# Kernel optimization log

Hardware: AMD Instinct MI355X
Metric: run time of the kernel (lower is better)

## Reference

```python
import jax, jax.numpy as jnp
import numpy as np

B, C, H, W = 1, 1, 1024, 1024
NP = 16                    # n_patches
S = NP * NP                # 256 tokens
D = 2048                   # hidden_d
NH = 16                    # heads
DH = D // NH               # 128
MLP = 4 * D
NB = 2                     # blocks
INPUT_D = C * (H // NP) * (W // NP)  # 4096
EPS = 1e-5


def positional_embeddings(s, d):
    # result[i,j] = sin(i/10000**(j/d)) if j even else cos(i/10000**((j-1)/d))
    i = jnp.arange(s, dtype=jnp.float32)[:, None]
    j = jnp.arange(d, dtype=jnp.float32)[None, :]
    even = (jnp.arange(d) % 2 == 0)[None, :]
    expo = jnp.where(even, j, j - 1.0) / d
    ang = i / (10000.0 ** expo)
    return jnp.where(even, jnp.sin(ang), jnp.cos(ang))


def layer_norm(x, g, b):
    m = x.mean(-1, keepdims=True)
    v = ((x - m) ** 2).mean(-1, keepdims=True)
    return (x - m) / jnp.sqrt(v + EPS) * g + b


def setup_inputs() -> dict:
    key = jax.random.key(0)
    ks = jax.random.split(key, 20)
    s = 0.02
    return {
        "images": jax.random.normal(ks[0], (B, C, H, W), jnp.float32),
        "memory": jax.random.normal(ks[1], (1, 8), jnp.float32),
        "wmap": jax.random.normal(ks[2], (INPUT_D, D), jnp.float32) * s,
        "bmap": jnp.zeros((D,), jnp.float32),
        "ln1_g": jnp.ones((NB, D), jnp.float32),
        "ln1_b": jnp.zeros((NB, D), jnp.float32),
        "qw": jax.random.normal(ks[3], (NB, NH, DH, DH), jnp.float32) * s,
        "qb": jnp.zeros((NB, NH, DH), jnp.float32),
        "kw": jax.random.normal(ks[4], (NB, NH, DH, DH), jnp.float32) * s,
        "kb": jnp.zeros((NB, NH, DH), jnp.float32),
        "vw": jax.random.normal(ks[5], (NB, NH, DH, DH), jnp.float32) * s,
        "vb": jnp.zeros((NB, NH, DH), jnp.float32),
        "ln2_g": jnp.ones((NB, D), jnp.float32),
        "ln2_b": jnp.zeros((NB, D), jnp.float32),
        "w1": jax.random.normal(ks[6], (NB, D, MLP), jnp.float32) * s,
        "b1": jnp.zeros((NB, MLP), jnp.float32),
        "w2": jax.random.normal(ks[7], (NB, MLP, D), jnp.float32) * s,
        "b2": jnp.zeros((NB, D), jnp.float32),
        "head_w": jax.random.normal(ks[8], (D, 1), jnp.float32) * s,
        "head_b": jnp.zeros((1,), jnp.float32),
    }


def reference(images, memory, wmap, bmap, ln1_g, ln1_b, qw, qb, kw, kb, vw, vb,
              ln2_g, ln2_b, w1, b1, w2, b2, head_w, head_b):
    # patchify: view(1, n_patches**2, num_h*num_v) -> (1, 256, 4096)
    patches = images.reshape(1, S, INPUT_D)
    tokens = patches @ wmap + bmap                      # (1, S, D)
    x = tokens + positional_embeddings(S, D)
    scale = DH ** 0.5
    for l in range(NB):
        h = layer_norm(x, ln1_g[l], ln1_b[l])
        h4 = h.reshape(B, S, NH, DH)
        q = jnp.einsum('bshd,hde->bshe', h4, qw[l]) + qb[l]
        k = jnp.einsum('bshd,hde->bshe', h4, kw[l]) + kb[l]
        v = jnp.einsum('bshd,hde->bshe', h4, vw[l]) + vb[l]
        att = jax.nn.softmax(jnp.einsum('bshe,bthe->bhst', q, k) / scale, axis=-1)
        attn_out = jnp.einsum('bhst,bthe->bshe', att, v).reshape(B, S, D)
        x = x + attn_out
        h2 = layer_norm(x, ln2_g[l], ln2_b[l])
        x = x + (jax.nn.gelu(h2 @ w1[l] + b1[l], approximate=False) @ w2[l] + b2[l])
    cls = x[:, 0]                                       # (1, D)
    out = jax.nn.sigmoid(cls @ head_w + head_b)         # (1, 1)
    return (out, memory)
```

## Files before the change

kernel.cpp:

```cpp
#include <hip/hip_runtime.h>
#include <math.h>

#define SQ   256
#define DD   2048
#define NHD  16
#define DHD  128
#define MLPD 8192
#define KIN  4096
#define INV_SQRT_DH 0.08838834764831845f

typedef __attribute__((ext_vector_type(8))) short bf16x8;
typedef __attribute__((ext_vector_type(4))) float f32x4;

__device__ __forceinline__ float gelu_f(float x) {
    return 0.5f * x * (1.0f + erff(x * 0.70710678118654752f));
}

__device__ __forceinline__ short f2bf(float f) {
    unsigned u = __float_as_uint(f);
    unsigned r = (u + 0x7fffu + ((u >> 16) & 1u)) >> 16;
    return (short)r;
}

__global__ __launch_bounds__(256) void gemm_splitk(const float* __restrict__ A,
                                                   const float* __restrict__ W,
                                                   float* __restrict__ C,
                                                   int N, int K, int KC) {
    __shared__ short As[64 * 64];
    __shared__ short Bs[64 * 64];
    const int tid = threadIdx.x;
    const int n0 = blockIdx.x * 64, m0 = blockIdx.y * 64;
    const int kstart = blockIdx.z * KC;
    const int wv = tid >> 6, ln = tid & 63;
    const int l15 = ln & 15, q = ln >> 4;

    f32x4 acc[4];
    #pragma unroll
    for (int j = 0; j < 4; j++) acc[j] = (f32x4){0.f, 0.f, 0.f, 0.f};

    const int am = tid >> 2, akb = (tid & 3) * 16, ac0 = (tid & 3) * 2;
    const int bn = tid & 63, bkb = (tid >> 6) * 16, bc0 = (tid >> 6) * 2;
    short* as0 = &As[am * 64 + ((ac0 ^ (am & 7)) * 8)];
    short* as1 = &As[am * 64 + (((ac0 + 1) ^ (am & 7)) * 8)];
    short* bs0 = &Bs[bn * 64 + ((bc0 ^ (bn & 7)) * 8)];
    short* bs1 = &Bs[bn * 64 + (((bc0 + 1) ^ (bn & 7)) * 8)];
    const int arow = 16 * wv + l15;
    const short* af0 = &As[arow * 64 + ((q ^ (arow & 7)) * 8)];
    const short* af1 = &As[arow * 64 + (((q + 4) ^ (arow & 7)) * 8)];

    for (int kc = kstart; kc < kstart + KC; kc += 64) {
        const float* ap = A + (size_t)(m0 + am) * K + kc + akb;
        float4 a0 = *(const float4*)ap;
        float4 a1 = *(const float4*)(ap + 4);
        float4 a2 = *(const float4*)(ap + 8);
        float4 a3 = *(const float4*)(ap + 12);
        const float* wp = W + (size_t)(kc + bkb) * N + n0 + bn;
        float wb[16];
        #pragma unroll
        for (int j = 0; j < 16; j++) wb[j] = wp[(size_t)j * N];

        __syncthreads();
        {
            short t[16] = {f2bf(a0.x), f2bf(a0.y), f2bf(a0.z), f2bf(a0.w),
                           f2bf(a1.x), f2bf(a1.y), f2bf(a1.z), f2bf(a1.w),
                           f2bf(a2.x), f2bf(a2.y), f2bf(a2.z), f2bf(a2.w),
                           f2bf(a3.x), f2bf(a3.y), f2bf(a3.z), f2bf(a3.w)};
            *(bf16x8*)as0 = *(bf16x8*)&t[0];
            *(bf16x8*)as1 = *(bf16x8*)&t[8];
            short u[16];
            #pragma unroll
            for (int j = 0; j < 16; j++) u[j] = f2bf(wb[j]);
            *(bf16x8*)bs0 = *(bf16x8*)&u[0];
            *(bf16x8*)bs1 = *(bf16x8*)&u[8];
        }
        __syncthreads();

        bf16x8 fa0 = *(const bf16x8*)af0;
        bf16x8 fa1 = *(const bf16x8*)af1;
        #pragma unroll
        for (int jt = 0; jt < 4; jt++) {
            const int brow = 16 * jt + l15;
            bf16x8 fb0 = *(const bf16x8*)&Bs[brow * 64 + ((q ^ (brow & 7)) * 8)];
            bf16x8 fb1 = *(const bf16x8*)&Bs[brow * 64 + (((q + 4) ^ (brow & 7)) * 8)];
            acc[jt] = __builtin_amdgcn_mfma_f32_16x16x32_bf16(fa0, fb0, acc[jt], 0, 0, 0);
            acc[jt] = __builtin_amdgcn_mfma_f32_16x16x32_bf16(fa1, fb1, acc[jt], 0, 0, 0);
        }
    }
    #pragma unroll
    for (int jt = 0; jt < 4; jt++) {
        const int n = n0 + 16 * jt + l15;
        #pragma unroll
        for (int i = 0; i < 4; i++) {
            const int m = m0 + 16 * wv + q * 4 + i;
            atomicAdd(&C[(size_t)m * N + n], acc[jt][i]);
        }
    }
}

__global__ __launch_bounds__(256) void epi_pos(float* __restrict__ x,
                                               const float* __restrict__ bmap) {
    const int idx = blockIdx.x * 256 + threadIdx.x;
    const int m = idx >> 11, n = idx & 2047;
    float val = x[idx] + bmap[n];
    float jf = (float)n;
    float expo = ((n & 1) ? (jf - 1.0f) : jf) * (1.0f / 2048.0f);
    float ang = (float)m * powf(10000.0f, -expo);
    x[idx] = val + ((n & 1) ? cosf(ang) : sinf(ang));
}

__global__ __launch_bounds__(256) void epi_gelu(float* __restrict__ y,
                                                const float* __restrict__ b1) {
    const int idx = blockIdx.x * 256 + threadIdx.x;
    y[idx] = gelu_f(y[idx] + b1[idx & 8191]);
}

__global__ __launch_bounds__(256) void epi_bias(float* __restrict__ x,
                                                const float* __restrict__ b2) {
    const int idx = blockIdx.x * 256 + threadIdx.x;
    x[idx] += b2[idx & 2047];
}

__global__ __launch_bounds__(256) void qkv_mfma(const float* __restrict__ h,
                                                const float* __restrict__ qw, const float* __restrict__ kw,
                                                const float* __restrict__ vw, const float* __restrict__ qb,
                                                const float* __restrict__ kb, const float* __restrict__ vb,
                                                float* __restrict__ q, float* __restrict__ k,
                                                float* __restrict__ v) {
    __shared__ short As[64 * 64];
    __shared__ short Bs[64 * 64];
    const int head = blockIdx.x, m0 = blockIdx.y * 64;
    const int type = blockIdx.z >> 1, n0 = (blockIdx.z & 1) * 64;
    const float* W; const float* B; float* O;
    if (type == 0)      { W = qw; B = qb; O = q; }
    else if (type == 1) { W = kw; B = kb; O = k; }
    else                { W = vw; B = vb; O = v; }
    W += (size_t)head * DHD * DHD;
    B += head * DHD;
    const int hoff = head * DHD;
    const int tid = threadIdx.x;
    const int wv = tid >> 6, ln = tid & 63;
    const int l15 = ln & 15, qq = ln >> 4;

    f32x4 acc[4];
    #pragma unroll
    for (int j = 0; j < 4; j++) acc[j] = (f32x4){0.f, 0.f, 0.f, 0.f};

    const int am = tid >> 2, akb = (tid & 3) * 16, ac0 = (tid & 3) * 2;
    const int bn = tid & 63, bkb = (tid >> 6) * 16, bc0 = (tid >> 6) * 2;
    short* as0 = &As[am * 64 + ((ac0 ^ (am & 7)) * 8)];
    short* as1 = &As[am * 64 + (((ac0 + 1) ^ (am & 7)) * 8)];
    short* bs0 = &Bs[bn * 64 + ((bc0 ^ (bn & 7)) * 8)];
    short* bs1 = &Bs[bn * 64 + (((bc0 + 1) ^ (bn & 7)) * 8)];
    const int arow = 16 * wv + l15;
    const short* af0 = &As[arow * 64 + ((qq ^ (arow & 7)) * 8)];
    const short* af1 = &As[arow * 64 + (((qq + 4) ^ (arow & 7)) * 8)];

    for (int kc = 0; kc < DHD; kc += 64) {
        const float* ap = h + (size_t)(m0 + am) * DD + hoff + kc + akb;
        float4 a0 = *(const float4*)ap;
        float4 a1 = *(const float4*)(ap + 4);
        float4 a2 = *(const float4*)(ap + 8);
        float4 a3 = *(const float4*)(ap + 12);
        const float* wp = W + (size_t)(kc + bkb) * DHD + n0 + bn;
        float wb[16];
        #pragma unroll
        for (int j = 0; j < 16; j++) wb[j] = wp[j * DHD];

        __syncthreads();
        {
            short t[16] = {f2bf(a0.x), f2bf(a0.y), f2bf(a0.z), f2bf(a0.w),
                           f2bf(a1.x), f2bf(a1.y), f2bf(a1.z), f2bf(a1.w),
                           f2bf(a2.x), f2bf(a2.y), f2bf(a2.z), f2bf(a2.w),
                           f2bf(a3.x), f2bf(a3.y), f2bf(a3.z), f2bf(a3.w)};
            *(bf16x8*)as0 = *(bf16x8*)&t[0];
            *(bf16x8*)as1 = *(bf16x8*)&t[8];
            short u[16];
            #pragma unroll
            for (int j = 0; j < 16; j++) u[j] = f2bf(wb[j]);
            *(bf16x8*)bs0 = *(bf16x8*)&u[0];
            *(bf16x8*)bs1 = *(bf16x8*)&u[8];
        }
        __syncthreads();

        bf16x8 fa0 = *(const bf16x8*)af0;
        bf16x8 fa1 = *(const bf16x8*)af1;
        #pragma unroll
        for (int jt = 0; jt < 4; jt++) {
            const int brow = 16 * jt + l15;
            bf16x8 fb0 = *(const bf16x8*)&Bs[brow * 64 + ((qq ^ (brow & 7)) * 8)];
            bf16x8 fb1 = *(const bf16x8*)&Bs[brow * 64 + (((qq + 4) ^ (brow & 7)) * 8)];
            acc[jt] = __builtin_amdgcn_mfma_f32_16x16x32_bf16(fa0, fb0, acc[jt], 0, 0, 0);
            acc[jt] = __builtin_amdgcn_mfma_f32_16x16x32_bf16(fa1, fb1, acc[jt], 0, 0, 0);
        }
    }
    #pragma unroll
    for (int jt = 0; jt < 4; jt++) {
        const int n = n0 + 16 * jt + l15;
        #pragma unroll
        for (int i = 0; i < 4; i++) {
            const int m = m0 + 16 * wv + qq * 4 + i;
            O[(size_t)m * DD + hoff + n] = acc[jt][i] + B[n];
        }
    }
}

__global__ __launch_bounds__(256) void ln_kernel(const float* __restrict__ xin,
                                                 const float* __restrict__ g,
                                                 const float* __restrict__ b,
                                                 float* __restrict__ out,
                                                 float* __restrict__ zbuf, int zn) {
    __shared__ float red[8];
    const int tid = threadIdx.x;
    for (int i = tid; i < zn; i += 256) zbuf[i] = 0.0f;
    const int row = blockIdx.x;
    const float* xr = xin + row * DD;
    float vals[8];
    float s = 0.0f;
    #pragma unroll
    for (int i = 0; i < 8; i++) { vals[i] = xr[tid + i * 256]; s += vals[i]; }
    #pragma unroll
    for (int o = 32; o > 0; o >>= 1) s += __shfl_down(s, o);
    if ((tid & 63) == 0) red[tid >> 6] = s;
    __syncthreads();
    if (tid == 0) red[4] = (red[0] + red[1] + red[2] + red[3]) * (1.0f / 2048.0f);
    __syncthreads();
    const float mean = red[4];
    float vs = 0.0f;
    #pragma unroll
    for (int i = 0; i < 8; i++) { float d = vals[i] - mean; vs += d * d; }
    #pragma unroll
    for (int o = 32; o > 0; o >>= 1) vs += __shfl_down(vs, o);
    if ((tid & 63) == 0) red[tid >> 6] = vs;
    __syncthreads();
    if (tid == 0) red[5] = rsqrtf((red[0] + red[1] + red[2] + red[3]) * (1.0f / 2048.0f) + 1e-5f);
    __syncthreads();
    const float inv = red[5];
    #pragma unroll
    for (int i = 0; i < 8; i++) {
        int c = tid + i * 256;
        out[row * DD + c] = (vals[i] - mean) * inv * g[c] + b[c];
    }
}

__global__ __launch_bounds__(256) void attn_kernel(const float* __restrict__ q,
                                                   const float* __restrict__ k,
                                                   const float* __restrict__ v,
                                                   float* __restrict__ x) {
    __shared__ float qs[16][129];
    __shared__ float ks[32][129];
    __shared__ float ps[16][257];
    const int head = blockIdx.x, r0 = blockIdx.y * 16;
    const int tid = threadIdx.x, hoff = head * DHD;
    for (int i = tid; i < 16 * 128; i += 256) {
        int r = i >> 7, d = i & 127;
        qs[r][d] = q[(r0 + r) * DD + hoff + d];
    }
    for (int jt = 0; jt < 256; jt += 32) {
        __syncthreads();
        for (int i = tid; i < 32 * 128; i += 256) {
            int r = i >> 7, d = i & 127;
            ks[r][d] = k[(jt + r) * DD + hoff + d];
        }
        __syncthreads();
        #pragma unroll
        for (int idx = tid; idx < 16 * 32; idx += 256) {
            int i = idx >> 5, j = idx & 31;
            float s = 0.0f;
            #pragma unroll
            for (int d = 0; d < 128; d++) s += qs[i][d] * ks[j][d];
            ps[i][jt + j] = s * INV_SQRT_DH;
        }
    }
    __syncthreads();
    if (tid < 16) {
        float mx = -1e30f;
        for (int j = 0; j < 256; j++) mx = fmaxf(mx, ps[tid][j]);
        float sm = 0.0f;
        for (int j = 0; j < 256; j++) { float e = __expf(ps[tid][j] - mx); ps[tid][j] = e; sm += e; }
        float inv = 1.0f / sm;
        for (int j = 0; j < 256; j++) ps[tid][j] *= inv;
    }
    __syncthreads();
    for (int idx = tid; idx < 16 * 128; idx += 256) {
        int i = idx >> 7, e = idx & 127;
        float acc = 0.0f;
        #pragma unroll 8
        for (int j = 0; j < 256; j++) acc += ps[i][j] * v[j * DD + hoff + e];
        x[(r0 + i) * DD + hoff + e] += acc;
    }
}

__global__ __launch_bounds__(256) void attn0_kernel(const float* __restrict__ q,
                                                    const float* __restrict__ k,
                                                    const float* __restrict__ v,
                                                    float* __restrict__ x) {
    __shared__ float q0[128];
    __shared__ float p[256];
    __shared__ float red[8];
    const int h = blockIdx.x, tid = threadIdx.x, hoff = h * DHD;
    if (tid < 128) q0[tid] = q[hoff + tid];
    __syncthreads();
    const float* kr = k + tid * DD + hoff;
    float s = 0.0f;
    #pragma unroll 8
    for (int d = 0; d < 128; d++) s += q0[d] * kr[d];
    s *= INV_SQRT_DH;
    float m = s;
    #pragma unroll
    for (int o = 32; o > 0; o >>= 1) m = fmaxf(m, __shfl_down(m, o));
    if ((tid & 63) == 0) red[tid >> 6] = m;
    __syncthreads();
    if (tid == 0) red[4] = fmaxf(fmaxf(red[0], red[1]), fmaxf(red[2], red[3]));
    __syncthreads();
    const float mx = red[4];
    float e = __expf(s - mx);
    p[tid] = e;
    float t = e;
    #pragma unroll
    for (int o = 32; o > 0; o >>= 1) t += __shfl_down(t, o);
    if ((tid & 63) == 0) red[tid >> 6] = t;
    __syncthreads();
    if (tid == 0) red[5] = red[0] + red[1] + red[2] + red[3];
    __syncthreads();
    const float inv = 1.0f / red[5];
    if (tid < 128) {
        float acc = 0.0f;
        #pragma unroll 8
        for (int j = 0; j < 256; j++) acc += p[j] * v[j * DD + hoff + tid];
        x[hoff + tid] += acc * inv;
    }
}

__global__ __launch_bounds__(256) void gemv1_kernel(const float* __restrict__ h2,
                                                    const float* __restrict__ w1,
                                                    float* __restrict__ y) {
    const int n = blockIdx.x * 256 + threadIdx.x;
    const int k0 = blockIdx.y * 256;
    float s = 0.0f;
    #pragma unroll 8
    for (int k = 0; k < 256; k++) s += h2[k0 + k] * w1[(size_t)(k0 + k) * MLPD + n];
    atomicAdd(&y[n], s);
}

__global__ __launch_bounds__(256) void gelu_bias_kernel(float* __restrict__ y,
                                                        const float* __restrict__ b1) {
    const int n = blockIdx.x * 256 + threadIdx.x;
    y[n] = gelu_f(y[n] + b1[n]);
}

__global__ __launch_bounds__(256) void gemv2_kernel(const float* __restrict__ y1,
                                                    const float* __restrict__ w2,
                                                    float* __restrict__ x) {
    const int m = blockIdx.x * 256 + threadIdx.x;
    const int k0 = blockIdx.y * 512;
    float s = 0.0f;
    #pragma unroll 8
    for (int k = 0; k < 512; k++) s += y1[k0 + k] * w2[(size_t)(k0 + k) * DD + m];
    atomicAdd(&x[m], s);
}

__global__ __launch_bounds__(256) void head_kernel(const float* __restrict__ x,
                                                   const float* __restrict__ b2l,
                                                   const float* __restrict__ hw,
                                                   const float* __restrict__ hb,
                                                   const float* __restrict__ mem,
                                                   float* __restrict__ out) {
    __shared__ float red[8];
    const int tid = threadIdx.x;
    float s = 0.0f;
    for (int m = tid; m < 2048; m += 256) s += (x[m] + b2l[m]) * hw[m];
    #pragma unroll
    for (int o = 32; o > 0; o >>= 1) s += __shfl_down(s, o);
    if ((tid & 63) == 0) red[tid >> 6] = s;
    __syncthreads();
    if (tid == 0) {
        float t = red[0] + red[1] + red[2] + red[3];
        out[0] = 1.0f / (1.0f + __expf(-(t + hb[0])));
    }
    if (tid < 8) out[1 + tid] = mem[tid];
}

extern "C" void kernel_launch(void* const* d_in, const int* in_sizes, int n_in,
                              void* d_out, int out_size, void* d_ws, size_t ws_size,
                              hipStream_t stream) {
    const float* images = (const float*)d_in[0];
    const float* memory = (const float*)d_in[1];
    const float* wmap   = (const float*)d_in[2];
    const float* bmap   = (const float*)d_in[3];
    const float* ln1_g  = (const float*)d_in[4];
    const float* ln1_b  = (const float*)d_in[5];
    const float* qw     = (const float*)d_in[6];
    const float* qb     = (const float*)d_in[7];
    const float* kw     = (const float*)d_in[8];
    const float* kb     = (const float*)d_in[9];
    const float* vw     = (const float*)d_in[10];
    const float* vb     = (const float*)d_in[11];
    const float* ln2_g  = (const float*)d_in[12];
    const float* ln2_b  = (const float*)d_in[13];
    const float* w1     = (const float*)d_in[14];
    const float* b1     = (const float*)d_in[15];
    const float* w2     = (const float*)d_in[16];
    const float* b2     = (const float*)d_in[17];
    const float* head_w = (const float*)d_in[18];
    const float* head_b = (const float*)d_in[19];
    float* out = (float*)d_out;

    float* ws = (float*)d_ws;
    float* x     = ws;
    float* h     = x + SQ * DD;
    float* q     = h + SQ * DD;
    float* k     = q + SQ * DD;
    float* v     = k + SQ * DD;
    float* y1    = v + SQ * DD;
    float* y1row = y1 + SQ * MLPD;
    float* h2row = y1row + MLPD;

    hipMemsetAsync(x, 0, (size_t)SQ * DD * sizeof(float), stream);
    gemm_splitk<<<dim3(DD / 64, SQ / 64, 8), 256, 0, stream>>>(images, wmap, x, DD, KIN, 512);
    epi_pos<<<SQ * DD / 256, 256, 0, stream>>>(x, bmap);

    for (int l = 0; l < 2; l++) {
        const size_t wofs = (size_t)l * NHD * DHD * DHD;
        const size_t bofs = (size_t)l * NHD * DHD;
        ln_kernel<<<SQ, 256, 0, stream>>>(x, ln1_g + l * DD, ln1_b + l * DD, h, nullptr, 0);
        qkv_mfma<<<dim3(NHD, SQ / 64, 6), 256, 0, stream>>>(h, qw + wofs, kw + wofs, vw + wofs,
                                                            qb + bofs, kb + bofs, vb + bofs,
                                                            q, k, v);
        if (l == 0) {
            attn_kernel<<<dim3(NHD, SQ / 16), 256, 0, stream>>>(q, k, v, x);
            ln_kernel<<<SQ, 256, 0, stream>>>(x, ln2_g, ln2_b, h, nullptr, 0);
            hipMemsetAsync(y1, 0, (size_t)SQ * MLPD * sizeof(float), stream);
            gemm_splitk<<<dim3(MLPD / 64, SQ / 64, 2), 256, 0, stream>>>(h, w1, y1, MLPD, DD, 1024);
            epi_gelu<<<SQ * MLPD / 256, 256, 0, stream>>>(y1, b1);
            gemm_splitk<<<dim3(DD / 64, SQ / 64, 8), 256, 0, stream>>>(y1, w2, x, DD, MLPD, 1024);
            epi_bias<<<SQ * DD / 256, 256, 0, stream>>>(x, b2);
        } else {
            attn0_kernel<<<NHD, 256, 0, stream>>>(q, k, v, x);
            ln_kernel<<<1, 256, 0, stream>>>(x, ln2_g + DD, ln2_b + DD, h2row, y1row, MLPD);
            gemv1_kernel<<<dim3(MLPD / 256, 8), 256, 0, stream>>>(h2row, w1 + (size_t)DD * MLPD, y1row);
            gelu_bias_kernel<<<MLPD / 256, 256, 0, stream>>>(y1row, b1 + MLPD);
            gemv2_kernel<<<dim3(DD / 256, 16), 256, 0, stream>>>(y1row, w2 + (size_t)DD * MLPD, x);
            head_kernel<<<1, 256, 0, stream>>>(x, b2 + DD, head_w, head_b, memory, out);
        }
    }
}
```

Measured before the change: 616.1 us.

## Rewrite layer-0 attention with bf16 MFMA and widen split-K for last-layer GEMVs

Replaces the scalar FP32 layer-0 attention kernel with an MFMA-based kernel. It converts Q, K, V and P to bf16, keeps the score tile in registers, applies softmax with wave shuffles, and uses swizzled shared memory for K, V^T and P. Separately, the last-layer GEMV kernels get more split-K blocks (32 instead of 8 or 16) to raise parallelism when streaming the large weight matrices. The cost is reduced precision in attention and more atomic adds.

```diff
diff --git a/kernel.cpp b/kernel.cpp
--- a/kernel.cpp
+++ b/kernel.cpp
@@ -204,6 +204,139 @@
     }
 }
 
+__global__ __launch_bounds__(256) void attn_mfma(const float* __restrict__ q,
+                                                 const float* __restrict__ k,
+                                                 const float* __restrict__ v,
+                                                 float* __restrict__ x) {
+    __shared__ short P[64 * 272];
+    __shared__ short ST[9216];
+    const int head = blockIdx.y, r0 = blockIdx.x * 64;
+    const int hoff = head * DHD;
+    const int tid = threadIdx.x;
+    const int wv = tid >> 6, ln = tid & 63;
+    const int l15 = ln & 15, qd = ln >> 4;
+
+    bf16x8 af[4];
+    {
+        const float* qp = q + (size_t)(r0 + 16 * wv + l15) * DD + hoff + qd * 8;
+        #pragma unroll
+        for (int s = 0; s < 4; s++) {
+            float4 f0 = *(const float4*)(qp + s * 32);
+            float4 f1 = *(const float4*)(qp + s * 32 + 4);
+            short t[8] = {f2bf(f0.x), f2bf(f0.y), f2bf(f0.z), f2bf(f0.w),
+                          f2bf(f1.x), f2bf(f1.y), f2bf(f1.z), f2bf(f1.w)};
+            af[s] = *(bf16x8*)t;
+        }
+    }
+
+    f32x4 sacc[16];
+    #pragma unroll
+    for (int i = 0; i < 16; i++) sacc[i] = (f32x4){0.f, 0.f, 0.f, 0.f};
+
+    const int skey = tid >> 2, scol = (tid & 3) * 32;
+    for (int kq = 0; kq < 4; kq++) {
+        const float* kp = k + (size_t)(kq * 64 + skey) * DD + hoff + scol;
+        float4 f[8];
+        #pragma unroll
+        for (int a = 0; a < 8; a++) f[a] = *(const float4*)(kp + a * 4);
+        if (kq) __syncthreads();
+        #pragma unroll
+        for (int a = 0; a < 4; a++) {
+            short t[8] = {f2bf(f[2*a].x), f2bf(f[2*a].y), f2bf(f[2*a].z), f2bf(f[2*a].w),
+                          f2bf(f[2*a+1].x), f2bf(f[2*a+1].y), f2bf(f[2*a+1].z), f2bf(f[2*a+1].w)};
+            *(bf16x8*)&ST[skey * 136 + scol + a * 8] = *(bf16x8*)t;
+        }
+        __syncthreads();
+        #pragma unroll
+        for (int nl = 0; nl < 4; nl++) {
+            #pragma unroll
+            for (int s = 0; s < 4; s++) {
+                bf16x8 bfr = *(const bf16x8*)&ST[(nl * 16 + l15) * 136 + s * 32 + qd * 8];
+                sacc[kq * 4 + nl] = __builtin_amdgcn_mfma_f32_16x16x32_bf16(af[s], bfr, sacc[kq * 4 + nl], 0, 0, 0);
+            }
+        }
+    }
+
+    float inv_s[4];
+    #pragma unroll
+    for (int i = 0; i < 4; i++) {
+        float m = -1e30f;
+        #pragma unroll
+        for (int nt = 0; nt < 16; nt++) m = fmaxf(m, sacc[nt][i]);
+        m = fmaxf(m, __shfl_xor(m, 1));
+        m = fmaxf(m, __shfl_xor(m, 2));
+        m = fmaxf(m, __shfl_xor(m, 4));
+        m = fmaxf(m, __shfl_xor(m, 8));
+        float sum = 0.f;
+        #pragma unroll
+        for (int nt = 0; nt < 16; nt++) {
+            float e = __expf((sacc[nt][i] - m) * INV_SQRT_DH);
+            sacc[nt][i] = e;
+            sum += e;
+        }
+        sum += __shfl_xor(sum, 1);
+        sum += __shfl_xor(sum, 2);
+        sum += __shfl_xor(sum, 4);
+        sum += __shfl_xor(sum, 8);
+        inv_s[i] = 1.0f / sum;
+    }
+    #pragma unroll
+    for (int nt = 0; nt < 16; nt++) {
+        const int col = nt * 16 + l15;
+        const int chunk = col >> 3, c7 = col & 7;
+        #pragma unroll
+        for (int i = 0; i < 4; i++) {
+            const int row = 16 * wv + 4 * qd + i;
+            P[row * 272 + ((chunk ^ (row & 7)) * 8) + c7] = f2bf(sacc[nt][i] * inv_s[i]);
+        }
+    }
+    __syncthreads();
+
+    f32x4 oacc[8];
+    #pragma unroll
+    for (int e = 0; e < 8; e++) oacc[e] = (f32x4){0.f, 0.f, 0.f, 0.f};
+
+    const int ve = tid & 127, vks = (tid >> 7) * 32;
+    for (int kq = 0; kq < 4; kq++) {
+        float vv[32];
+        #pragma unroll
+        for (int j = 0; j < 32; j++)
+            vv[j] = v[(size_t)(kq * 64 + vks + j) * DD + hoff + ve];
+        if (kq) __syncthreads();
+        #pragma unroll
+        for (int c = 0; c < 4; c++) {
+            short t[8];
+            #pragma unroll
+            for (int b = 0; b < 8; b++) t[b] = f2bf(vv[c * 8 + b]);
+            const int ch = (vks >> 3) + c;
+            *(bf16x8*)&ST[ve * 72 + ((ch ^ (ve & 7)) * 8)] = *(bf16x8*)t;
+        }
+        __syncthreads();
+        #pragma unroll
+        for (int s = 0; s < 2; s++) {
+            const int row = 16 * wv + l15;
+            const int pc = kq * 8 + s * 4 + qd;
+            bf16x8 pa = *(const bf16x8*)&P[row * 272 + ((pc ^ (row & 7)) * 8)];
+            #pragma unroll
+            for (int et = 0; et < 8; et++) {
+                const int er = et * 16 + l15;
+                const int vc = s * 4 + qd;
+                bf16x8 vb = *(const bf16x8*)&ST[er * 72 + ((vc ^ (er & 7)) * 8)];
+                oacc[et] = __builtin_amdgcn_mfma_f32_16x16x32_bf16(pa, vb, oacc[et], 0, 0, 0);
+            }
+        }
+    }
+    #pragma unroll
+    for (int et = 0; et < 8; et++) {
+        const int e = et * 16 + l15;
+        #pragma unroll
+        for (int i = 0; i < 4; i++) {
+            const int row = r0 + 16 * wv + 4 * qd + i;
+            x[(size_t)row * DD + hoff + e] += oacc[et][i];
+        }
+    }
+}
+
 __global__ __launch_bounds__(256) void ln_kernel(const float* __restrict__ xin,
                                                  const float* __restrict__ g,
                                                  const float* __restrict__ b,
@@ -242,54 +375,6 @@
     }
 }
 
-__global__ __launch_bounds__(256) void attn_kernel(const float* __restrict__ q,
-                                                   const float* __restrict__ k,
-                                                   const float* __restrict__ v,
-                                                   float* __restrict__ x) {
-    __shared__ float qs[16][129];
-    __shared__ float ks[32][129];
-    __shared__ float ps[16][257];
-    const int head = blockIdx.x, r0 = blockIdx.y * 16;
-    const int tid = threadIdx.x, hoff = head * DHD;
-    for (int i = tid; i < 16 * 128; i += 256) {
-        int r = i >> 7, d = i & 127;
-        qs[r][d] = q[(r0 + r) * DD + hoff + d];
-    }
-    for (int jt = 0; jt < 256; jt += 32) {
-        __syncthreads();
-        for (int i = tid; i < 32 * 128; i += 256) {
-            int r = i >> 7, d = i & 127;
-            ks[r][d] = k[(jt + r) * DD + hoff + d];
-        }
-        __syncthreads();
-        #pragma unroll
-        for (int idx = tid; idx < 16 * 32; idx += 256) {
-            int i = idx >> 5, j = idx & 31;
-            float s = 0.0f;
-            #pragma unroll
-            for (int d = 0; d < 128; d++) s += qs[i][d] * ks[j][d];
-            ps[i][jt + j] = s * INV_SQRT_DH;
-        }
-    }
-    __syncthreads();
-    if (tid < 16) {
-        float mx = -1e30f;
-        for (int j = 0; j < 256; j++) mx = fmaxf(mx, ps[tid][j]);
-        float sm = 0.0f;
-        for (int j = 0; j < 256; j++) { float e = __expf(ps[tid][j] - mx); ps[tid][j] = e; sm += e; }
-        float inv = 1.0f / sm;
-        for (int j = 0; j < 256; j++) ps[tid][j] *= inv;
-    }
-    __syncthreads();
-    for (int idx = tid; idx < 16 * 128; idx += 256) {
-        int i = idx >> 7, e = idx & 127;
-        float acc = 0.0f;
-        #pragma unroll 8
-        for (int j = 0; j < 256; j++) acc += ps[i][j] * v[j * DD + hoff + e];
-        x[(r0 + i) * DD + hoff + e] += acc;
-    }
-}
-
 __global__ __launch_bounds__(256) void attn0_kernel(const float* __restrict__ q,
                                                     const float* __restrict__ k,
                                                     const float* __restrict__ v,
@@ -335,10 +420,10 @@
                                                     const float* __restrict__ w1,
                                                     float* __restrict__ y) {
     const int n = blockIdx.x * 256 + threadIdx.x;
-    const int k0 = blockIdx.y * 256;
+    const int k0 = blockIdx.y * 64;
     float s = 0.0f;
     #pragma unroll 8
-    for (int k = 0; k < 256; k++) s += h2[k0 + k] * w1[(size_t)(k0 + k) * MLPD + n];
+    for (int k = 0; k < 64; k++) s += h2[k0 + k] * w1[(size_t)(k0 + k) * MLPD + n];
     atomicAdd(&y[n], s);
 }
 
@@ -352,10 +437,10 @@
                                                     const float* __restrict__ w2,
                                                     float* __restrict__ x) {
     const int m = blockIdx.x * 256 + threadIdx.x;
-    const int k0 = blockIdx.y * 512;
+    const int k0 = blockIdx.y * 256;
     float s = 0.0f;
     #pragma unroll 8
-    for (int k = 0; k < 512; k++) s += y1[k0 + k] * w2[(size_t)(k0 + k) * DD + m];
+    for (int k = 0; k < 256; k++) s += y1[k0 + k] * w2[(size_t)(k0 + k) * DD + m];
     atomicAdd(&x[m], s);
 }
 
@@ -427,7 +512,7 @@
                                                             qb + bofs, kb + bofs, vb + bofs,
                                                             q, k, v);
         if (l == 0) {
-            attn_kernel<<<dim3(NHD, SQ / 16), 256, 0, stream>>>(q, k, v, x);
+            attn_mfma<<<dim3(SQ / 64, NHD), 256, 0, stream>>>(q, k, v, x);
             ln_kernel<<<SQ, 256, 0, stream>>>(x, ln2_g, ln2_b, h, nullptr, 0);
             hipMemsetAsync(y1, 0, (size_t)SQ * MLPD * sizeof(float), stream);
             gemm_splitk<<<dim3(MLPD / 64, SQ / 64, 2), 256, 0, stream>>>(h, w1, y1, MLPD, DD, 1024);
@@ -437,9 +522,9 @@
         } else {
             attn0_kernel<<<NHD, 256, 0, stream>>>(q, k, v, x);
             ln_kernel<<<1, 256, 0, stream>>>(x, ln2_g + DD, ln2_b + DD, h2row, y1row, MLPD);
-            gemv1_kernel<<<dim3(MLPD / 256, 8), 256, 0, stream>>>(h2row, w1 + (size_t)DD * MLPD, y1row);
+            gemv1_kernel<<<dim3(MLPD / 256, 32), 256, 0, stream>>>(h2row, w1 + (size_t)DD * MLPD, y1row);
             gelu_bias_kernel<<<MLPD / 256, 256, 0, stream>>>(y1row, b1 + MLPD);
-            gemv2_kernel<<<dim3(DD / 256, 16), 256, 0, stream>>>(y1row, w2 + (size_t)DD * MLPD, x);
+            gemv2_kernel<<<dim3(DD / 256, 32), 256, 0, stream>>>(y1row, w2 + (size_t)DD * MLPD, x);
             head_kernel<<<1, 256, 0, stream>>>(x, b2 + DD, head_w, head_b, memory, out);
         }
     }
```

Result: faster. 507.6 us (-17.6%).
